# Kernel optimization log

Hardware: AMD Instinct MI355X
Metric: run time of the kernel (lower is better)

## Reference

```python
import jax, jax.numpy as jnp
import numpy as np

B, T, E = 8, 2048, 2048  # T must equal head_size == n_embd (see source constraints)
H = 1
HS = E // H
FF = 4 * E


def _init(key, shape, scale=0.02):
    return (jax.random.normal(key, shape, jnp.float32) * scale).astype(jnp.float32)


def setup_inputs() -> dict:
    key = jax.random.key(0)
    ks = jax.random.split(key, 10)
    return {
        "x": jax.random.normal(ks[0], (B, T, E), jnp.float32),
        "gamma1": jnp.ones((E,), jnp.float32),
        "beta1": jnp.zeros((E,), jnp.float32),
        "Wq": _init(ks[1], (HS, E)),   # torch Linear weight layout [out, in]
        "Wk": _init(ks[2], (HS, E)),
        "Wv": _init(ks[3], (HS, E)),
        "Wo": _init(ks[4], (HS, H * HS)),
        "bo": jnp.zeros((HS,), jnp.float32),
        "gamma2": jnp.ones((E,), jnp.float32),
        "beta2": jnp.zeros((E,), jnp.float32),
        "W1": _init(ks[5], (FF, E)),
        "b1": jnp.zeros((FF,), jnp.float32),
        "W2": _init(ks[6], (E, FF)),
        "b2": jnp.zeros((E,), jnp.float32),
    }


def _layernorm(x, gamma, beta, eps=1e-5):
    mu = jnp.mean(x, axis=-1, keepdims=True)
    var = jnp.mean(jnp.square(x - mu), axis=-1, keepdims=True)
    return (x - mu) * jax.lax.rsqrt(var + eps) * gamma + beta


def reference(x, gamma1, beta1, Wq, Wk, Wv, Wo, bo, gamma2, beta2, W1, b1, W2, b2):
    # --- multi-head (n_head=1) causal self-attention on LN(x) ---
    h = _layernorm(x, gamma1, beta1)                      # [B,T,E]
    q = jnp.einsum('bte,he->bth', h, Wq)                  # [B,T,HS]
    k = jnp.einsum('bte,he->bth', h, Wk)
    v = jnp.einsum('bte,he->bth', h, Wv)
    # scale by sqrt(C) where C = x channel dim = n_embd (as in source)
    wei = jnp.einsum('bth,bsh->bts', q, k) / jnp.sqrt(jnp.float32(E))
    mask = jnp.tril(jnp.ones((T, T), bool))               # full tril buffer
    wei = jnp.where(mask, wei, -jnp.inf)
    wei = jax.nn.softmax(wei, axis=-1)
    attn = jnp.einsum('bts,bsh->bth', wei, v)             # [B,T,HS]
    attn = jnp.einsum('bth,oh->bto', attn, Wo) + bo       # output proj [B,T,HS]
    x = x + attn                                          # residual (HS == E)
    # --- feed-forward on LN(x) ---
    h2 = _layernorm(x, gamma2, beta2)
    ff = jax.nn.relu(jnp.einsum('bte,fe->btf', h2, W1) + b1)
    ff = jnp.einsum('btf,ef->bte', ff, W2) + b2
    return x + ff
```

## Files before the change

### kernel.cpp

```cpp
#include <hip/hip_runtime.h>
#include <cstdint>

typedef __bf16 bf16;
typedef __bf16 bf16x8 __attribute__((ext_vector_type(8)));
typedef float f32x4 __attribute__((ext_vector_type(4)));

#define B_  8
#define T_  2048
#define E_  2048
#define FF_ 8192
#define M_  (B_ * T_)

__device__ __forceinline__ void gload_lds16(const void* g, void* l) {
    __builtin_amdgcn_global_load_lds(
        (const __attribute__((address_space(1))) uint32_t*)(uintptr_t)g,
        (__attribute__((address_space(3))) uint32_t*)(uintptr_t)l,
        16, 0, 0);
}

__global__ __launch_bounds__(256) void cvt_kernel(const float* __restrict__ src,
                                                  bf16* __restrict__ dst, int n8) {
    int i = blockIdx.x * 256 + threadIdx.x;
    if (i >= n8) return;
    const float4* s = (const float4*)src + (size_t)i * 2;
    float4 a = s[0], b = s[1];
    bf16x8 o;
    o[0] = (bf16)a.x; o[1] = (bf16)a.y; o[2] = (bf16)a.z; o[3] = (bf16)a.w;
    o[4] = (bf16)b.x; o[5] = (bf16)b.y; o[6] = (bf16)b.z; o[7] = (bf16)b.w;
    *(bf16x8*)&dst[(size_t)i * 8] = o;
}

__global__ __launch_bounds__(256) void ln_kernel(const float* __restrict__ x,
                                                 const float* __restrict__ gamma,
                                                 const float* __restrict__ beta,
                                                 bf16* __restrict__ out) {
    int row = blockIdx.x;
    int tid = threadIdx.x;
    const float* xr = x + (size_t)row * E_;
    float4 v0 = *(const float4*)&xr[tid * 8];
    float4 v1 = *(const float4*)&xr[tid * 8 + 4];
    float xs[8] = {v0.x, v0.y, v0.z, v0.w, v1.x, v1.y, v1.z, v1.w};
    float s = 0.f, s2 = 0.f;
#pragma unroll
    for (int j = 0; j < 8; j++) { s += xs[j]; s2 += xs[j] * xs[j]; }
#pragma unroll
    for (int o = 32; o > 0; o >>= 1) { s += __shfl_xor(s, o); s2 += __shfl_xor(s2, o); }
    __shared__ float red[8];
    int wave = tid >> 6, lane = tid & 63;
    if (lane == 0) { red[wave] = s; red[4 + wave] = s2; }
    __syncthreads();
    s  = red[0] + red[1] + red[2] + red[3];
    s2 = red[4] + red[5] + red[6] + red[7];
    float mean = s * (1.0f / E_);
    float var  = s2 * (1.0f / E_) - mean * mean;
    float rstd = rsqrtf(var + 1e-5f);
    float4 g0 = *(const float4*)&gamma[tid * 8];
    float4 g1 = *(const float4*)&gamma[tid * 8 + 4];
    float4 b0 = *(const float4*)&beta[tid * 8];
    float4 b1 = *(const float4*)&beta[tid * 8 + 4];
    float gs[8] = {g0.x, g0.y, g0.z, g0.w, g1.x, g1.y, g1.z, g1.w};
    float bs[8] = {b0.x, b0.y, b0.z, b0.w, b1.x, b1.y, b1.z, b1.w};
    bf16x8 o;
#pragma unroll
    for (int j = 0; j < 8; j++)
        o[j] = (bf16)((xs[j] - mean) * rstd * gs[j] + bs[j]);
    *(bf16x8*)&out[(size_t)row * E_ + tid * 8] = o;
}

__global__ __launch_bounds__(256) void softmax_kernel(bf16* __restrict__ S) {
    int row = blockIdx.x;
    int b = row >> 11;
    int t = row & (T_ - 1);
    bf16* p = S + (size_t)b * T_ * T_ + (size_t)t * T_;
    int L = t + 1;
    int Lpad = ((t >> 7) + 1) << 7;
    int tid = threadIdx.x;
    int wave = tid >> 6, lane = tid & 63;
    float v[8];
    float m = -3.0e38f;
#pragma unroll
    for (int j = 0; j < 8; j++) {
        int s = tid + j * 256;
        v[j] = (s < L) ? (float)p[s] : -3.0e38f;
        m = fmaxf(m, v[j]);
    }
#pragma unroll
    for (int o = 32; o > 0; o >>= 1) m = fmaxf(m, __shfl_xor(m, o));
    __shared__ float red[8];
    if (lane == 0) red[wave] = m;
    __syncthreads();
    m = fmaxf(fmaxf(red[0], red[1]), fmaxf(red[2], red[3]));
    float sum = 0.f;
#pragma unroll
    for (int j = 0; j < 8; j++) {
        int s = tid + j * 256;
        float e = (s < L) ? __expf(v[j] - m) : 0.f;
        v[j] = e;
        sum += e;
    }
#pragma unroll
    for (int o = 32; o > 0; o >>= 1) sum += __shfl_xor(sum, o);
    if (lane == 0) red[4 + wave] = sum;
    __syncthreads();
    sum = red[4] + red[5] + red[6] + red[7];
    float inv = 1.0f / sum;
#pragma unroll
    for (int j = 0; j < 8; j++) {
        int s = tid + j * 256;
        if (s < Lpad) p[s] = (bf16)(v[j] * inv);
    }
}

template <int MODE>
__global__ __launch_bounds__(256) void gemm_bt(
    const bf16* __restrict__ A, const bf16* __restrict__ B,
    int K, int lda, int ldb, int ldc,
    long sA, long sB, long sC,
    void* __restrict__ Cv,
    const float* __restrict__ bias,
    const float* __restrict__ resid,
    float scale, int flags) {
    constexpr int BM = 128, BN = 128, BK = 32;
    int bz = blockIdx.z;
    int tm, tn;
    if (MODE == 1 || MODE == 3) {
        tm = blockIdx.x; tn = blockIdx.y;
    } else {
        int p = blockIdx.x + gridDim.x * blockIdx.y;
        int per = 32 * gridDim.y;
        int grp = p / per;
        int rem = p - grp * per;
        tm = grp * 32 + (rem & 31);
        tn = rem >> 5;
    }
    if (MODE == 1 && tn > tm) return;

    __shared__ bf16 As[BM * BK];
    __shared__ bf16 Bs[BN * BK];

    const int tid = threadIdx.x;
    const int wave = tid >> 6, lane = tid & 63;
    const int l15 = lane & 15, quad = lane >> 4;
    const int wm = wave >> 1, wn = wave & 1;

    const bf16* Ab = A + sA * bz + (size_t)tm * BM * lda;
    const bf16* Bb = B + sB * bz + (size_t)tn * BN * ldb;

    int Keff = K;
    if (MODE == 3) Keff = min(K, (tm + 1) * BM);

    f32x4 acc[4][4];
#pragma unroll
    for (int i = 0; i < 4; i++)
#pragma unroll
        for (int j = 0; j < 4; j++) { acc[i][j][0] = 0.f; acc[i][j][1] = 0.f; acc[i][j][2] = 0.f; acc[i][j][3] = 0.f; }

    const int srow = wave * 16 + (lane >> 2);
    const int scol = (lane & 3) * 8;

    for (int k0 = 0; k0 < Keff; k0 += BK) {
#pragma unroll
        for (int u = 0; u < 2; u++) {
            gload_lds16(Ab + (size_t)(u * 64 + srow) * lda + k0 + scol,
                        &As[(u * 64 + wave * 16) * BK]);
            gload_lds16(Bb + (size_t)(u * 64 + srow) * ldb + k0 + scol,
                        &Bs[(u * 64 + wave * 16) * BK]);
        }
        __syncthreads();
        bf16x8 af[4], bF[4];
#pragma unroll
        for (int mi = 0; mi < 4; mi++)
            af[mi] = *(const bf16x8*)&As[(wm * 64 + mi * 16 + l15) * BK + quad * 8];
#pragma unroll
        for (int ni = 0; ni < 4; ni++)
            bF[ni] = *(const bf16x8*)&Bs[(wn * 64 + ni * 16 + l15) * BK + quad * 8];
#pragma unroll
        for (int mi = 0; mi < 4; mi++)
#pragma unroll
            for (int ni = 0; ni < 4; ni++)
                acc[mi][ni] = __builtin_amdgcn_mfma_f32_16x16x32_bf16(af[mi], bF[ni], acc[mi][ni], 0, 0, 0);
        __syncthreads();
    }

    const int rb = tm * BM + wm * 64;
    const int cb = tn * BN + wn * 64;

    if (MODE == 1 || MODE == 3) {
        bf16* C = (bf16*)Cv + sC * bz;
#pragma unroll
        for (int mi = 0; mi < 4; mi++)
#pragma unroll
            for (int r = 0; r < 4; r++) {
                int row = rb + mi * 16 + quad * 4 + r;
#pragma unroll
                for (int ni = 0; ni < 4; ni++) {
                    int col = cb + ni * 16 + l15;
                    float v = acc[mi][ni][r];
                    if (MODE == 1) v *= scale;
                    C[(size_t)row * ldc + col] = (bf16)v;
                }
            }
    }
}

template <int MODE>
__global__ __launch_bounds__(512, 2) void gemm256(
    const bf16* __restrict__ A, const bf16* __restrict__ B,
    int K, int lda, int ldb, int ldc,
    void* __restrict__ Cv,
    const float* __restrict__ bias,
    const float* __restrict__ resid,
    int flags) {
    __shared__ bf16 lds[2][2][2][2][4096];

    const int tid  = threadIdx.x;
    const int lane = tid & 63;
    const int l15  = lane & 15, quad = lane >> 4;
    const int wave = tid >> 6;
    const int wm = wave >> 2;
    const int wn = wave & 3;
    const int bh = wn >> 1, bq = wn & 1;

    int p   = blockIdx.x + gridDim.x * blockIdx.y;
    int nwg = gridDim.x * gridDim.y;
    int cpx = nwg >> 3;
    int w   = (p & 7) * cpx + (p >> 3);
    int tn_ = w % gridDim.y;
    int tm_ = w / gridDim.y;

    const int NT = K >> 6;

    int d    = tid * 16;
    int lsw  = d ^ ((d >> 4) & 0x30);
    int srow = lsw >> 6;
    int ske  = (lsw & 63) >> 1;
    int wq   = wave * 1024;

    const bf16* As0 = A + (size_t)(tm_ * 256 + srow) * lda + ske;
    const bf16* As1 = As0 + (size_t)128 * lda;
    const bf16* Bs0 = B + (size_t)(tn_ * 256 + srow) * ldb + ske;
    const bf16* Bs1 = Bs0 + (size_t)128 * ldb;

    const int roff = (l15 * 64 + quad * 16) ^ ((l15 & 12) << 2);

    f32x4 acc[8][4];
#pragma unroll
    for (int i = 0; i < 8; i++)
#pragma unroll
        for (int j = 0; j < 4; j++) {
            acc[i][j][0] = 0.f; acc[i][j][1] = 0.f; acc[i][j][2] = 0.f; acc[i][j][3] = 0.f;
        }

    bf16x8 bfr[4];

#define STG(P0, P1, CB, R0, R1)                                                        \
    do {                                                                               \
        gload_lds16((P0) + (CB), (char*)(R0) + wq);                                    \
        gload_lds16((P1) + (CB), (char*)(R1) + wq);                                    \
    } while (0)

    STG(As0, As1, 0,  &lds[0][0][0][0][0], &lds[0][0][1][0][0]);
    STG(Bs0, Bs1, 0,  &lds[0][1][0][0][0], &lds[0][1][1][0][0]);
    STG(As0, As1, 32, &lds[0][0][0][1][0], &lds[0][0][1][1][0]);
    STG(Bs0, Bs1, 32, &lds[0][1][0][1][0], &lds[0][1][1][1][0]);
    STG(As0, As1, 64, &lds[1][0][0][0][0], &lds[1][0][1][0][0]);
    STG(Bs0, Bs1, 64, &lds[1][1][0][0][0], &lds[1][1][1][0][0]);
    asm volatile("s_waitcnt vmcnt(8)" ::: "memory");
    __builtin_amdgcn_s_barrier();

#define PH(Q, KK, H, DOB, SP0, SP1, SCB, SR0, SR1, DOVM)                               \
    do {                                                                               \
        const char* ar_ = (const char*)&lds[(Q)][0][wm][(KK)][0] + (H) * 4096 + roff;  \
        bf16x8 a_[4];                                                                  \
        _Pragma("unroll")                                                              \
        for (int mi = 0; mi < 4; mi++)                                                 \
            a_[mi] = *(const bf16x8*)(ar_ + mi * 1024);                                \
        if (DOB) {                                                                     \
            const char* br_ = (const char*)&lds[(Q)][1][bh][(KK)][0] + bq * 4096 + roff; \
            _Pragma("unroll")                                                          \
            for (int ni = 0; ni < 4; ni++)                                             \
                bfr[ni] = *(const bf16x8*)(br_ + ni * 1024);                           \
        }                                                                              \
        STG(SP0, SP1, SCB, SR0, SR1);                                                  \
        __builtin_amdgcn_s_barrier();                                                  \
        __builtin_amdgcn_s_setprio(1);                                                 \
        _Pragma("unroll")                                                              \
        for (int mi = 0; mi < 4; mi++)                                                 \
            _Pragma("unroll")                                                          \
            for (int ni = 0; ni < 4; ni++)                                             \
                acc[(H) * 4 + mi][ni] = __builtin_amdgcn_mfma_f32_16x16x32_bf16(       \
                    a_[mi], bfr[ni], acc[(H) * 4 + mi][ni], 0, 0, 0);                  \
        __builtin_amdgcn_s_setprio(0);                                                 \
        if (DOVM) asm volatile("s_waitcnt vmcnt(8)" ::: "memory");                     \
        __builtin_amdgcn_s_barrier();                                                  \
    } while (0)

#define TILE(Q, WS1, WS2)                                                                              \
    do {                                                                                               \
        PH(Q, 0, 0, 1, As0, As1, (WS1) * 64 + 32, &lds[(Q) ^ 1][0][0][1][0], &lds[(Q) ^ 1][0][1][1][0], 0); \
        PH(Q, 0, 1, 0, Bs0, Bs1, (WS1) * 64 + 32, &lds[(Q) ^ 1][1][0][1][0], &lds[(Q) ^ 1][1][1][1][0], 1); \
        PH(Q, 1, 0, 1, As0, As1, (WS2) * 64, &lds[(Q)][0][0][0][0], &lds[(Q)][0][1][0][0], 0);         \
        PH(Q, 1, 1, 0, Bs0, Bs1, (WS2) * 64, &lds[(Q)][1][0][0][0], &lds[(Q)][1][1][0][0], 1);         \
    } while (0)

    for (int t = 0; t < NT; t += 2) {
        int wa = t + 1;
        int wb = (t + 2 < NT) ? t + 2 : NT - 1;
        int wd = (t + 3 < NT) ? t + 3 : NT - 1;
        TILE(0, wa, wb);
        TILE(1, wb, wd);
    }
    asm volatile("s_waitcnt vmcnt(0)" ::: "memory");

#undef TILE
#undef PH
#undef STG

    const int rb0 = tm_ * 256 + wm * 128;
    const int cb0 = tn_ * 256 + wn * 64;
    if (MODE == 4) {
        float* C = (float*)Cv;
#pragma unroll
        for (int mf = 0; mf < 8; mf++)
#pragma unroll
            for (int r = 0; r < 4; r++) {
                int row = rb0 + mf * 16 + quad * 4 + r;
#pragma unroll
                for (int nf = 0; nf < 4; nf++) {
                    int col = cb0 + nf * 16 + l15;
                    size_t idx = (size_t)row * ldc + col;
                    C[idx] = acc[mf][nf][r] + bias[col] + resid[idx];
                }
            }
    } else if (MODE == 5) {
        bf16* C = (bf16*)Cv;
#pragma unroll
        for (int mf = 0; mf < 8; mf++)
#pragma unroll
            for (int r = 0; r < 4; r++) {
                int row = rb0 + mf * 16 + quad * 4 + r;
#pragma unroll
                for (int nf = 0; nf < 4; nf++) {
                    int col = cb0 + nf * 16 + l15;
                    float v = acc[mf][nf][r] + bias[col];
                    C[(size_t)row * ldc + col] = (bf16)fmaxf(v, 0.f);
                }
            }
    } else if (MODE == 6) {
        float* C = (float*)Cv;
#pragma unroll
        for (int mf = 0; mf < 8; mf++)
#pragma unroll
            for (int r = 0; r < 4; r++) {
                int row = rb0 + mf * 16 + quad * 4 + r;
#pragma unroll
                for (int nf = 0; nf < 4; nf++) {
                    int col = cb0 + nf * 16 + l15;
                    size_t idx = (size_t)row * ldc + col;
                    float v = acc[mf][nf][r];
                    if (flags) v += bias[col];
                    C[idx] = C[idx] + v;
                }
            }
    }
}

__global__ __launch_bounds__(256) void gemm_qkv(
    const bf16* __restrict__ A, const bf16* __restrict__ B,
    bf16* __restrict__ q, bf16* __restrict__ k, bf16* __restrict__ vt) {
    constexpr int BM = 128, BN = 128, BK = 32;
    int p = blockIdx.x + gridDim.x * blockIdx.y;
    int per = 32 * gridDim.y;
    int grp = p / per;
    int rem = p - grp * per;
    int tm = grp * 32 + (rem & 31);
    int tn = rem >> 5;

    __shared__ bf16 As[BM * BK];
    __shared__ bf16 Bs[BN * BK];
    __shared__ bf16 Tb[64 * 136];

    const int tid = threadIdx.x;
    const int wave = tid >> 6, lane = tid & 63;
    const int l15 = lane & 15, quad = lane >> 4;
    const int wm = wave >> 1, wn = wave & 1;

    const bf16* Ab = A + (size_t)tm * BM * E_;
    const bf16* Bb = B + (size_t)tn * BN * E_;

    f32x4 acc[4][4];
#pragma unroll
    for (int i = 0; i < 4; i++)
#pragma unroll
        for (int j = 0; j < 4; j++) { acc[i][j][0] = 0.f; acc[i][j][1] = 0.f; acc[i][j][2] = 0.f; acc[i][j][3] = 0.f; }

    const int srow = wave * 16 + (lane >> 2);
    const int scol = (lane & 3) * 8;

    for (int k0 = 0; k0 < E_; k0 += BK) {
#pragma unroll
        for (int u = 0; u < 2; u++) {
            gload_lds16(Ab + (size_t)(u * 64 + srow) * E_ + k0 + scol,
                        &As[(u * 64 + wave * 16) * BK]);
            gload_lds16(Bb + (size_t)(u * 64 + srow) * E_ + k0 + scol,
                        &Bs[(u * 64 + wave * 16) * BK]);
        }
        __syncthreads();
        bf16x8 af[4], bF[4];
#pragma unroll
        for (int mi = 0; mi < 4; mi++)
            af[mi] = *(const bf16x8*)&As[(wm * 64 + mi * 16 + l15) * BK + quad * 8];
#pragma unroll
        for (int ni = 0; ni < 4; ni++)
            bF[ni] = *(const bf16x8*)&Bs[(wn * 64 + ni * 16 + l15) * BK + quad * 8];
#pragma unroll
        for (int mi = 0; mi < 4; mi++)
#pragma unroll
            for (int ni = 0; ni < 4; ni++)
                acc[mi][ni] = __builtin_amdgcn_mfma_f32_16x16x32_bf16(af[mi], bF[ni], acc[mi][ni], 0, 0, 0);
        __syncthreads();
    }

    if (tn < 32) {
        bf16* C = (tn < 16) ? q : k;
        int cb = ((tn & 15) * BN) + wn * 64;
        int rbase = tm * BM + wm * 64;
#pragma unroll
        for (int mi = 0; mi < 4; mi++)
#pragma unroll
            for (int r = 0; r < 4; r++) {
                int row = rbase + mi * 16 + quad * 4 + r;
#pragma unroll
                for (int ni = 0; ni < 4; ni++) {
                    int col = cb + ni * 16 + l15;
                    C[(size_t)row * E_ + col] = (bf16)acc[mi][ni][r];
                }
            }
    } else {
        int b = tm >> 4;
        int tbase = (tm & 15) * 128;
        int nb = (tn - 32) * BN;
#pragma unroll
        for (int h = 0; h < 2; h++) {
            __syncthreads();
            if (wn == h) {
#pragma unroll
                for (int mi = 0; mi < 4; mi++)
#pragma unroll
                    for (int r = 0; r < 4; r++) {
                        int rl = wm * 64 + mi * 16 + quad * 4 + r;
#pragma unroll
                        for (int ni = 0; ni < 4; ni++) {
                            int cl = ni * 16 + l15;
                            Tb[cl * 136 + rl] = (bf16)acc[mi][ni][r];
                        }
                    }
            }
            __syncthreads();
#pragma unroll
            for (int pp = 0; pp < 4; pp++) {
                int cl = pp * 16 + (tid >> 4);
                int rch = (tid & 15) * 8;
                bf16x8 val = *(const bf16x8*)&Tb[cl * 136 + rch];
                int n = nb + h * 64 + cl;
                *(bf16x8*)&vt[(size_t)b * E_ * T_ + (size_t)n * T_ + tbase + rch] = val;
            }
        }
    }
}

extern "C" void kernel_launch(void* const* d_in, const int* in_sizes, int n_in,
                              void* d_out, int out_size, void* d_ws, size_t ws_size,
                              hipStream_t stream) {
    const float* x      = (const float*)d_in[0];
    const float* gamma1 = (const float*)d_in[1];
    const float* beta1  = (const float*)d_in[2];
    const float* Wq     = (const float*)d_in[3];
    const float* Wk     = (const float*)d_in[4];
    const float* Wv     = (const float*)d_in[5];
    const float* Wo     = (const float*)d_in[6];
    const float* bo     = (const float*)d_in[7];
    const float* gamma2 = (const float*)d_in[8];
    const float* beta2  = (const float*)d_in[9];
    const float* W1     = (const float*)d_in[10];
    const float* b1     = (const float*)d_in[11];
    const float* W2     = (const float*)d_in[12];
    const float* b2     = (const float*)d_in[13];
    float* out = (float*)d_out;

    char* ws = (char*)d_ws;
    const size_t SZ = (size_t)M_ * E_ * 2;
    bf16* hbf  = (bf16*)(ws + 0 * SZ);
    bf16* qbf  = (bf16*)(ws + 1 * SZ);
    bf16* kbf  = (bf16*)(ws + 2 * SZ);
    bf16* vt   = (bf16*)(ws + 3 * SZ);
    bf16* Sp   = (bf16*)(ws + 4 * SZ);
    bf16* attn = hbf;
    bf16* h2   = qbf;
    bf16* ffb  = kbf;
    size_t woff = 5 * SZ;
    bf16* Wqb = (bf16*)(ws + woff); woff += (size_t)E_ * E_ * 2;
    bf16* Wkb = (bf16*)(ws + woff); woff += (size_t)E_ * E_ * 2;
    bf16* Wvb = (bf16*)(ws + woff); woff += (size_t)E_ * E_ * 2;
    bf16* Wob = (bf16*)(ws + woff); woff += (size_t)E_ * E_ * 2;
    bf16* W1b = (bf16*)(ws + woff); woff += (size_t)FF_ * E_ * 2;
    bf16* W2b = (bf16*)(ws + woff); woff += (size_t)FF_ * E_ * 2;

    cvt_kernel<<<2048, 256, 0, stream>>>(Wq, Wqb, E_ * E_ / 8);
    cvt_kernel<<<2048, 256, 0, stream>>>(Wk, Wkb, E_ * E_ / 8);
    cvt_kernel<<<2048, 256, 0, stream>>>(Wv, Wvb, E_ * E_ / 8);
    cvt_kernel<<<2048, 256, 0, stream>>>(Wo, Wob, E_ * E_ / 8);
    cvt_kernel<<<8192, 256, 0, stream>>>(W1, W1b, FF_ * E_ / 8);
    cvt_kernel<<<8192, 256, 0, stream>>>(W2, W2b, FF_ * E_ / 8);

    ln_kernel<<<M_, 256, 0, stream>>>(x, gamma1, beta1, hbf);

    dim3 blk(256);
    dim3 blk512(512);
    dim3 gQKV(M_ / 128, 3 * E_ / 128, 1);
    gemm_qkv<<<gQKV, blk, 0, stream>>>(hbf, Wqb, qbf, kbf, vt);

    dim3 gAttn(T_ / 128, T_ / 128, B_);
    gemm_bt<1><<<gAttn, blk, 0, stream>>>(qbf, kbf, E_, E_, E_, T_,
                                          (long)T_ * E_, (long)T_ * E_, (long)T_ * T_,
                                          Sp, nullptr, nullptr, 0.022097086912079612f, 0);
    softmax_kernel<<<M_, 256, 0, stream>>>(Sp);
    gemm_bt<3><<<gAttn, blk, 0, stream>>>(Sp, vt, T_, T_, T_, E_,
                                          (long)T_ * T_, (long)E_ * T_, (long)T_ * E_,
                                          attn, nullptr, nullptr, 1.f, 0);
    dim3 gProj(M_ / 256, E_ / 256, 1);
    gemm256<4><<<gProj, blk512, 0, stream>>>(attn, Wob, E_, E_, E_, E_,
                                             out, bo, x, 0);
    ln_kernel<<<M_, 256, 0, stream>>>(out, gamma2, beta2, h2);
    dim3 gFF1(M_ / 256, 4096 / 256, 1);
    dim3 gFF2(M_ / 256, E_ / 256, 1);
    for (int s5 = 0; s5 < 2; s5++) {
        gemm256<5><<<gFF1, blk512, 0, stream>>>(h2, W1b + (size_t)s5 * 4096 * E_,
                                                E_, E_, E_, 4096,
                                                ffb, b1 + s5 * 4096, nullptr, 0);
        gemm256<6><<<gFF2, blk512, 0, stream>>>(ffb, W2b + s5 * 4096,
                                                4096, 4096, FF_, E_,
                                                out, b2, nullptr, s5 == 0 ? 1 : 0);
    }
}
```

Measured before the change: 2.824 ms.

## Route QKV and attention GEMMs through the 256x256 pipelined gemm256 kernel

Replaces the 128x128 single-buffered gemm_bt and gemm_qkv kernels with the larger 256x256 gemm256 kernel, extended with batch strides, causal tile skipping and a scale factor. The QKV projection now writes q, k and v into contiguous buffers, and a separate LDS transpose kernel produces v^T. Softmax padding is widened to 256 to match the new tile size. This trades an extra transpose pass and coarser causal granularity (more wasted work on the diagonal tiles) for better data reuse and pipelining in the dominant GEMMs.

```diff
diff --git a/kernel.cpp b/kernel.cpp
--- a/kernel.cpp
+++ b/kernel.cpp
@@ -73,7 +73,7 @@
     int t = row & (T_ - 1);
     bf16* p = S + (size_t)b * T_ * T_ + (size_t)t * T_;
     int L = t + 1;
-    int Lpad = ((t >> 7) + 1) << 7;
+    int Lpad = ((t >> 8) + 1) << 8;
     int tid = threadIdx.x;
     int wave = tid >> 6, lane = tid & 63;
     float v[8];
@@ -111,8 +111,32 @@
     }
 }
 
+__global__ __launch_bounds__(256) void transpose_kernel(const bf16* __restrict__ src,
+                                                        bf16* __restrict__ dst) {
+    __shared__ bf16 tb[64][72];
+    int b  = blockIdx.z;
+    int t0 = blockIdx.x * 64;
+    int h0 = blockIdx.y * 64;
+    const bf16* s = src + ((size_t)b * T_ + t0) * E_ + h0;
+    bf16* d = dst + ((size_t)b * E_ + h0) * T_ + t0;
+    int r  = threadIdx.x >> 3;
+    int c8 = (threadIdx.x & 7) * 8;
+#pragma unroll
+    for (int p = 0; p < 2; p++) {
+        bf16x8 v = *(const bf16x8*)&s[(size_t)(p * 32 + r) * E_ + c8];
+#pragma unroll
+        for (int j = 0; j < 8; j++) tb[c8 + j][p * 32 + r] = v[j];
+    }
+    __syncthreads();
+#pragma unroll
+    for (int p = 0; p < 2; p++) {
+        bf16x8 v = *(const bf16x8*)&tb[p * 32 + r][c8];
+        *(bf16x8*)&d[(size_t)(p * 32 + r) * T_ + c8] = v;
+    }
+}
+
 template <int MODE>
-__global__ __launch_bounds__(256) void gemm_bt(
+__global__ __launch_bounds__(512, 2) void gemm256(
     const bf16* __restrict__ A, const bf16* __restrict__ B,
     int K, int lda, int ldb, int ldc,
     long sA, long sB, long sC,
@@ -120,97 +144,6 @@
     const float* __restrict__ bias,
     const float* __restrict__ resid,
     float scale, int flags) {
-    constexpr int BM = 128, BN = 128, BK = 32;
-    int bz = blockIdx.z;
-    int tm, tn;
-    if (MODE == 1 || MODE == 3) {
-        tm = blockIdx.x; tn = blockIdx.y;
-    } else {
-        int p = blockIdx.x + gridDim.x * blockIdx.y;
-        int per = 32 * gridDim.y;
-        int grp = p / per;
-        int rem = p - grp * per;
-        tm = grp * 32 + (rem & 31);
-        tn = rem >> 5;
-    }
-    if (MODE == 1 && tn > tm) return;
-
-    __shared__ bf16 As[BM * BK];
-    __shared__ bf16 Bs[BN * BK];
-
-    const int tid = threadIdx.x;
-    const int wave = tid >> 6, lane = tid & 63;
-    const int l15 = lane & 15, quad = lane >> 4;
-    const int wm = wave >> 1, wn = wave & 1;
-
-    const bf16* Ab = A + sA * bz + (size_t)tm * BM * lda;
-    const bf16* Bb = B + sB * bz + (size_t)tn * BN * ldb;
-
-    int Keff = K;
-    if (MODE == 3) Keff = min(K, (tm + 1) * BM);
-
-    f32x4 acc[4][4];
-#pragma unroll
-    for (int i = 0; i < 4; i++)
-#pragma unroll
-        for (int j = 0; j < 4; j++) { acc[i][j][0] = 0.f; acc[i][j][1] = 0.f; acc[i][j][2] = 0.f; acc[i][j][3] = 0.f; }
-
-    const int srow = wave * 16 + (lane >> 2);
-    const int scol = (lane & 3) * 8;
-
-    for (int k0 = 0; k0 < Keff; k0 += BK) {
-#pragma unroll
-        for (int u = 0; u < 2; u++) {
-            gload_lds16(Ab + (size_t)(u * 64 + srow) * lda + k0 + scol,
-                        &As[(u * 64 + wave * 16) * BK]);
-            gload_lds16(Bb + (size_t)(u * 64 + srow) * ldb + k0 + scol,
-                        &Bs[(u * 64 + wave * 16) * BK]);
-        }
-        __syncthreads();
-        bf16x8 af[4], bF[4];
-#pragma unroll
-        for (int mi = 0; mi < 4; mi++)
-            af[mi] = *(const bf16x8*)&As[(wm * 64 + mi * 16 + l15) * BK + quad * 8];
-#pragma unroll
-        for (int ni = 0; ni < 4; ni++)
-            bF[ni] = *(const bf16x8*)&Bs[(wn * 64 + ni * 16 + l15) * BK + quad * 8];
-#pragma unroll
-        for (int mi = 0; mi < 4; mi++)
-#pragma unroll
-            for (int ni = 0; ni < 4; ni++)
-                acc[mi][ni] = __builtin_amdgcn_mfma_f32_16x16x32_bf16(af[mi], bF[ni], acc[mi][ni], 0, 0, 0);
-        __syncthreads();
-    }
-
-    const int rb = tm * BM + wm * 64;
-    const int cb = tn * BN + wn * 64;
-
-    if (MODE == 1 || MODE == 3) {
-        bf16* C = (bf16*)Cv + sC * bz;
-#pragma unroll
-        for (int mi = 0; mi < 4; mi++)
-#pragma unroll
-            for (int r = 0; r < 4; r++) {
-                int row = rb + mi * 16 + quad * 4 + r;
-#pragma unroll
-                for (int ni = 0; ni < 4; ni++) {
-                    int col = cb + ni * 16 + l15;
-                    float v = acc[mi][ni][r];
-                    if (MODE == 1) v *= scale;
-                    C[(size_t)row * ldc + col] = (bf16)v;
-                }
-            }
-    }
-}
-
-template <int MODE>
-__global__ __launch_bounds__(512, 2) void gemm256(
-    const bf16* __restrict__ A, const bf16* __restrict__ B,
-    int K, int lda, int ldb, int ldc,
-    void* __restrict__ Cv,
-    const float* __restrict__ bias,
-    const float* __restrict__ resid,
-    int flags) {
     __shared__ bf16 lds[2][2][2][2][4096];
 
     const int tid  = threadIdx.x;
@@ -221,14 +154,23 @@
     const int wn = wave & 3;
     const int bh = wn >> 1, bq = wn & 1;
 
-    int p   = blockIdx.x + gridDim.x * blockIdx.y;
-    int nwg = gridDim.x * gridDim.y;
-    int cpx = nwg >> 3;
-    int w   = (p & 7) * cpx + (p >> 3);
-    int tn_ = w % gridDim.y;
-    int tm_ = w / gridDim.y;
-
-    const int NT = K >> 6;
+    const int bz = blockIdx.z;
+    int tm_, tn_;
+    if (MODE == 1 || MODE == 3) {
+        tm_ = blockIdx.x; tn_ = blockIdx.y;
+        if (MODE == 1 && tn_ > tm_) return;
+    } else {
+        int p   = blockIdx.x + gridDim.x * blockIdx.y;
+        int nwg = gridDim.x * gridDim.y;
+        int cpx = nwg >> 3;
+        int w   = (p & 7) * cpx + (p >> 3);
+        tn_ = w % gridDim.y;
+        tm_ = w / gridDim.y;
+    }
+
+    int Keff = K;
+    if (MODE == 3) Keff = min(K, (tm_ + 1) * 256);
+    const int NT = Keff >> 6;
 
     int d    = tid * 16;
     int lsw  = d ^ ((d >> 4) & 0x30);
@@ -236,9 +178,9 @@
     int ske  = (lsw & 63) >> 1;
     int wq   = wave * 1024;
 
-    const bf16* As0 = A + (size_t)(tm_ * 256 + srow) * lda + ske;
+    const bf16* As0 = A + sA * bz + (size_t)(tm_ * 256 + srow) * lda + ske;
     const bf16* As1 = As0 + (size_t)128 * lda;
-    const bf16* Bs0 = B + (size_t)(tn_ * 256 + srow) * ldb + ske;
+    const bf16* Bs0 = B + sB * bz + (size_t)(tn_ * 256 + srow) * ldb + ske;
     const bf16* Bs1 = Bs0 + (size_t)128 * ldb;
 
     const int roff = (l15 * 64 + quad * 16) ^ ((l15 & 12) << 2);
@@ -318,7 +260,34 @@
 
     const int rb0 = tm_ * 256 + wm * 128;
     const int cb0 = tn_ * 256 + wn * 64;
-    if (MODE == 4) {
+    if (MODE == 1 || MODE == 3) {
+        bf16* C = (bf16*)Cv + sC * bz;
+#pragma unroll
+        for (int mf = 0; mf < 8; mf++)
+#pragma unroll
+            for (int r = 0; r < 4; r++) {
+                int row = rb0 + mf * 16 + quad * 4 + r;
+#pragma unroll
+                for (int nf = 0; nf < 4; nf++) {
+                    int col = cb0 + nf * 16 + l15;
+                    C[(size_t)row * ldc + col] = (bf16)(acc[mf][nf][r] * scale);
+                }
+            }
+    } else if (MODE == 7) {
+        bf16* C = (bf16*)Cv + (size_t)(cb0 >> 11) * M_ * E_;
+        int cB = cb0 & 2047;
+#pragma unroll
+        for (int mf = 0; mf < 8; mf++)
+#pragma unroll
+            for (int r = 0; r < 4; r++) {
+                int row = rb0 + mf * 16 + quad * 4 + r;
+#pragma unroll
+                for (int nf = 0; nf < 4; nf++) {
+                    int col = cB + nf * 16 + l15;
+                    C[(size_t)row * ldc + col] = (bf16)acc[mf][nf][r];
+                }
+            }
+    } else if (MODE == 4) {
         float* C = (float*)Cv;
 #pragma unroll
         for (int mf = 0; mf < 8; mf++)
@@ -362,110 +331,6 @@
                     C[idx] = C[idx] + v;
                 }
             }
-    }
-}
-
-__global__ __launch_bounds__(256) void gemm_qkv(
-    const bf16* __restrict__ A, const bf16* __restrict__ B,
-    bf16* __restrict__ q, bf16* __restrict__ k, bf16* __restrict__ vt) {
-    constexpr int BM = 128, BN = 128, BK = 32;
-    int p = blockIdx.x + gridDim.x * blockIdx.y;
-    int per = 32 * gridDim.y;
-    int grp = p / per;
-    int rem = p - grp * per;
-    int tm = grp * 32 + (rem & 31);
-    int tn = rem >> 5;
-
-    __shared__ bf16 As[BM * BK];
-    __shared__ bf16 Bs[BN * BK];
-    __shared__ bf16 Tb[64 * 136];
-
-    const int tid = threadIdx.x;
-    const int wave = tid >> 6, lane = tid & 63;
-    const int l15 = lane & 15, quad = lane >> 4;
-    const int wm = wave >> 1, wn = wave & 1;
-
-    const bf16* Ab = A + (size_t)tm * BM * E_;
-    const bf16* Bb = B + (size_t)tn * BN * E_;
-
-    f32x4 acc[4][4];
-#pragma unroll
-    for (int i = 0; i < 4; i++)
-#pragma unroll
-        for (int j = 0; j < 4; j++) { acc[i][j][0] = 0.f; acc[i][j][1] = 0.f; acc[i][j][2] = 0.f; acc[i][j][3] = 0.f; }
-
-    const int srow = wave * 16 + (lane >> 2);
-    const int scol = (lane & 3) * 8;
-
-    for (int k0 = 0; k0 < E_; k0 += BK) {
-#pragma unroll
-        for (int u = 0; u < 2; u++) {
-            gload_lds16(Ab + (size_t)(u * 64 + srow) * E_ + k0 + scol,
-                        &As[(u * 64 + wave * 16) * BK]);
-            gload_lds16(Bb + (size_t)(u * 64 + srow) * E_ + k0 + scol,
-                        &Bs[(u * 64 + wave * 16) * BK]);
-        }
-        __syncthreads();
-        bf16x8 af[4], bF[4];
-#pragma unroll
-        for (int mi = 0; mi < 4; mi++)
-            af[mi] = *(const bf16x8*)&As[(wm * 64 + mi * 16 + l15) * BK + quad * 8];
-#pragma unroll
-        for (int ni = 0; ni < 4; ni++)
-            bF[ni] = *(const bf16x8*)&Bs[(wn * 64 + ni * 16 + l15) * BK + quad * 8];
-#pragma unroll
-        for (int mi = 0; mi < 4; mi++)
-#pragma unroll
-            for (int ni = 0; ni < 4; ni++)
-                acc[mi][ni] = __builtin_amdgcn_mfma_f32_16x16x32_bf16(af[mi], bF[ni], acc[mi][ni], 0, 0, 0);
-        __syncthreads();
-    }
-
-    if (tn < 32) {
-        bf16* C = (tn < 16) ? q : k;
-        int cb = ((tn & 15) * BN) + wn * 64;
-        int rbase = tm * BM + wm * 64;
-#pragma unroll
-        for (int mi = 0; mi < 4; mi++)
-#pragma unroll
-            for (int r = 0; r < 4; r++) {
-                int row = rbase + mi * 16 + quad * 4 + r;
-#pragma unroll
-                for (int ni = 0; ni < 4; ni++) {
-                    int col = cb + ni * 16 + l15;
-                    C[(size_t)row * E_ + col] = (bf16)acc[mi][ni][r];
-                }
-            }
-    } else {
-        int b = tm >> 4;
-        int tbase = (tm & 15) * 128;
-        int nb = (tn - 32) * BN;
-#pragma unroll
-        for (int h = 0; h < 2; h++) {
-            __syncthreads();
-            if (wn == h) {
-#pragma unroll
-                for (int mi = 0; mi < 4; mi++)
-#pragma unroll
-                    for (int r = 0; r < 4; r++) {
-                        int rl = wm * 64 + mi * 16 + quad * 4 + r;
-#pragma unroll
-                        for (int ni = 0; ni < 4; ni++) {
-                            int cl = ni * 16 + l15;
-                            Tb[cl * 136 + rl] = (bf16)acc[mi][ni][r];
-                        }
-                    }
-            }
-            __syncthreads();
-#pragma unroll
-            for (int pp = 0; pp < 4; pp++) {
-                int cl = pp * 16 + (tid >> 4);
-                int rch = (tid & 15) * 8;
-                bf16x8 val = *(const bf16x8*)&Tb[cl * 136 + rch];
-                int n = nb + h * 64 + cl;
-                *(bf16x8*)&vt[(size_t)b * E_ * T_ + (size_t)n * T_ + tbase + rch] = val;
-            }
-        }
     }
 }
 
@@ -491,11 +356,12 @@
     char* ws = (char*)d_ws;
     const size_t SZ = (size_t)M_ * E_ * 2;
     bf16* hbf  = (bf16*)(ws + 0 * SZ);
+    bf16* vt   = (bf16*)(ws + 0 * SZ);
     bf16* qbf  = (bf16*)(ws + 1 * SZ);
     bf16* kbf  = (bf16*)(ws + 2 * SZ);
-    bf16* vt   = (bf16*)(ws + 3 * SZ);
+    bf16* vtmp = (bf16*)(ws + 3 * SZ);
     bf16* Sp   = (bf16*)(ws + 4 * SZ);
-    bf16* attn = hbf;
+    bf16* attn = vtmp;
     bf16* h2   = qbf;
     bf16* ffb  = kbf;
     size_t woff = 5 * SZ;
@@ -515,31 +381,33 @@
 
     ln_kernel<<<M_, 256, 0, stream>>>(x, gamma1, beta1, hbf);
 
-    dim3 blk(256);
     dim3 blk512(512);
-    dim3 gQKV(M_ / 128, 3 * E_ / 128, 1);
-    gemm_qkv<<<gQKV, blk, 0, stream>>>(hbf, Wqb, qbf, kbf, vt);
-
-    dim3 gAttn(T_ / 128, T_ / 128, B_);
-    gemm_bt<1><<<gAttn, blk, 0, stream>>>(qbf, kbf, E_, E_, E_, T_,
-                                          (long)T_ * E_, (long)T_ * E_, (long)T_ * T_,
-                                          Sp, nullptr, nullptr, 0.022097086912079612f, 0);
+    dim3 gQKV(M_ / 256, 3 * E_ / 256, 1);
+    gemm256<7><<<gQKV, blk512, 0, stream>>>(hbf, Wqb, E_, E_, E_, E_, 0, 0, 0,
+                                            qbf, nullptr, nullptr, 1.f, 0);
+    dim3 gT(T_ / 64, E_ / 64, B_);
+    transpose_kernel<<<gT, 256, 0, stream>>>(vtmp, vt);
+
+    dim3 gAttn(T_ / 256, T_ / 256, B_);
+    gemm256<1><<<gAttn, blk512, 0, stream>>>(qbf, kbf, E_, E_, E_, T_,
+                                             (long)T_ * E_, (long)T_ * E_, (long)T_ * T_,
+                                             Sp, nullptr, nullptr, 0.022097086912079612f, 0);
     softmax_kernel<<<M_, 256, 0, stream>>>(Sp);
-    gemm_bt<3><<<gAttn, blk, 0, stream>>>(Sp, vt, T_, T_, T_, E_,
-                                          (long)T_ * T_, (long)E_ * T_, (long)T_ * E_,
-                                          attn, nullptr, nullptr, 1.f, 0);
+    gemm256<3><<<gAttn, blk512, 0, stream>>>(Sp, vt, T_, T_, T_, E_,
+                                             (long)T_ * T_, (long)E_ * T_, (long)T_ * E_,
+                                             attn, nullptr, nullptr, 1.f, 0);
     dim3 gProj(M_ / 256, E_ / 256, 1);
-    gemm256<4><<<gProj, blk512, 0, stream>>>(attn, Wob, E_, E_, E_, E_,
-                                             out, bo, x, 0);
+    gemm256<4><<<gProj, blk512, 0, stream>>>(attn, Wob, E_, E_, E_, E_, 0, 0, 0,
+                                             out, bo, x, 1.f, 0);
     ln_kernel<<<M_, 256, 0, stream>>>(out, gamma2, beta2, h2);
     dim3 gFF1(M_ / 256, 4096 / 256, 1);
     dim3 gFF2(M_ / 256, E_ / 256, 1);
     for (int s5 = 0; s5 < 2; s5++) {
         gemm256<5><<<gFF1, blk512, 0, stream>>>(h2, W1b + (size_t)s5 * 4096 * E_,
-                                                E_, E_, E_, 4096,
-                                                ffb, b1 + s5 * 4096, nullptr, 0);
+                                                E_, E_, E_, 4096, 0, 0, 0,
+                                                ffb, b1 + s5 * 4096, nullptr, 1.f, 0);
         gemm256<6><<<gFF2, blk512, 0, stream>>>(ffb, W2b + s5 * 4096,
-                                                4096, 4096, FF_, E_,
-                                                out, b2, nullptr, s5 == 0 ? 1 : 0);
-    }
-}
+                                                4096, 4096, FF_, E_, 0, 0, 0,
+                                                out, b2, nullptr, 1.f, s5 == 0 ? 1 : 0);
+    }
+}
```

Result: faster. 2.461 ms (-12.9%).
